# Optimization experiments

Measured on AMD Instinct MI355X. Metric: run time of the kernel, lower is better.

## Reference

```python
import jax, jax.numpy as jnp
import numpy as np

N_NODES = 50000
N_EDGES = 1600000
IN_FEATS = 128
HIDDEN = 128
N_CLASSES = 16
N_GRAPHS = 512


def setup_inputs() -> dict:
    key = jax.random.key(0)
    ks = jax.random.split(key, 10)
    features = jax.random.normal(ks[0], (N_NODES, IN_FEATS), dtype=jnp.float32)
    src = jax.random.randint(ks[1], (N_EDGES,), 0, N_NODES, dtype=jnp.int32)
    dst = jax.random.randint(ks[2], (N_EDGES,), 0, N_NODES, dtype=jnp.int32)
    graph_ids = jnp.sort(jax.random.randint(ks[3], (N_NODES,), 0, N_GRAPHS, dtype=jnp.int32))
    # GraphConv weights (glorot-ish scaling) and biases
    W1 = jax.random.normal(ks[4], (IN_FEATS, HIDDEN), dtype=jnp.float32) / np.sqrt(IN_FEATS)
    b1 = jnp.zeros((HIDDEN,), dtype=jnp.float32)
    W2 = jax.random.normal(ks[5], (HIDDEN, HIDDEN), dtype=jnp.float32) / np.sqrt(HIDDEN)
    b2 = jnp.zeros((HIDDEN,), dtype=jnp.float32)
    Wf = jax.random.normal(ks[6], (HIDDEN, N_CLASSES), dtype=jnp.float32) / np.sqrt(HIDDEN)
    bf = jnp.zeros((N_CLASSES,), dtype=jnp.float32)
    return {"features": features, "W1": W1, "b1": b1, "W2": W2, "b2": b2,
            "Wf": Wf, "bf": bf, "src": src, "dst": dst, "graph_ids": graph_ids}


def _graph_conv(h, W, b, src, dst, norm_out, norm_in):
    # DGL GraphConv, norm='both': h' = D_in^{-1/2} * A^T * (D_out^{-1/2} * h) @ W + b
    h = h * norm_out[:, None]              # [N, d] scale by src out-degree
    agg = jax.ops.segment_sum(h[src], dst, num_segments=N_NODES)  # gather-scatter SpMM
    agg = agg * norm_in[:, None]
    return agg @ W + b


def reference(features, W1, b1, W2, b2, Wf, bf, src, dst, graph_ids):
    ones_e = jnp.ones((N_EDGES,), dtype=features.dtype)
    deg_out = jax.ops.segment_sum(ones_e, src, num_segments=N_NODES)
    deg_in = jax.ops.segment_sum(ones_e, dst, num_segments=N_NODES)
    norm_out = jnp.where(deg_out > 0, jax.lax.rsqrt(jnp.maximum(deg_out, 1.0)), 0.0)
    norm_in = jnp.where(deg_in > 0, jax.lax.rsqrt(jnp.maximum(deg_in, 1.0)), 0.0)

    x = jax.nn.relu(_graph_conv(features, W1, b1, src, dst, norm_out, norm_in))
    x = jax.nn.relu(_graph_conv(x, W2, b2, src, dst, norm_out, norm_in))

    # mean_nodes: per-graph mean pooling over batched graph
    sums = jax.ops.segment_sum(x, graph_ids, num_segments=N_GRAPHS)   # [G, d]
    counts = jax.ops.segment_sum(jnp.ones((N_NODES,), dtype=x.dtype), graph_ids,
                                 num_segments=N_GRAPHS)
    pooled = sums / jnp.maximum(counts, 1.0)[:, None]
    return pooled @ Wf + bf
```

## Files before the change

### kernel.cpp

```cpp
#include <hip/hip_runtime.h>

#define N_NODES 50000
#define N_EDGES 1600000
#define FEATS 128
#define N_GRAPHS 512
#define N_CLASSES 16

#define NC 400
#define CE 4000
#define NB 391
#define SLAB 4608
#define CSLAB 5632
#define ZROW 50000
#define SRC_MID 25000

typedef __attribute__((ext_vector_type(8))) short bf16x8;
typedef __attribute__((ext_vector_type(4))) float f32x4;

__device__ inline unsigned bf16_rne_bits(float x) {
    unsigned u = __float_as_uint(x);
    return (u + 0x7FFFu + ((u >> 16) & 1u)) >> 16;
}
__device__ inline unsigned pack_bf16(float a, float b) {
    return (bf16_rne_bits(b) << 16) | bf16_rne_bits(a);
}
__device__ inline float bf16lo(unsigned u) { return __uint_as_float(u << 16); }
__device__ inline float bf16hi(unsigned u) { return __uint_as_float(u & 0xFFFF0000u); }

__global__ __launch_bounds__(256) void countrank_kernel(
        const int* __restrict__ src, const int* __restrict__ dst,
        unsigned* __restrict__ cntD, unsigned* __restrict__ cntS,
        const float* __restrict__ W1, const float* __restrict__ W2,
        unsigned short* __restrict__ t1h, unsigned short* __restrict__ t1l,
        unsigned short* __restrict__ t2h, unsigned short* __restrict__ t2l,
        int* __restrict__ gboth) {
    __shared__ unsigned hD[NB], hS[NB];
    if (blockIdx.x >= NC) {
        int b = blockIdx.x - NC;
        if (b == 0) {
#pragma unroll
            for (int i = 0; i < 4; ++i) gboth[threadIdx.x + 256 * i] = 0;
        }
        const float* W = (b < 64) ? W1 : W2;
        unsigned short* th = (b < 64) ? t1h : t2h;
        unsigned short* tl = (b < 64) ? t1l : t2l;
        int idx = (b & 63) * 256 + threadIdx.x;
        int k = idx >> 7;
        int col = idx & 127;
        float w = W[idx];
        unsigned hb = bf16_rne_bits(w);
        float hf = __uint_as_float(hb << 16);
        unsigned lb = bf16_rne_bits(w - hf);
        th[col * 128 + k] = (unsigned short)hb;
        tl[col * 128 + k] = (unsigned short)lb;
        return;
    }
    for (int i = threadIdx.x; i < NB; i += 256) { hD[i] = 0; hS[i] = 0; }
    __syncthreads();
    int c = blockIdx.x;
    int lo = c * CE;
    for (int i = lo + threadIdx.x; i < lo + CE; i += 256) {
        atomicAdd(&hD[dst[i] >> 7], 1u);
        atomicAdd(&hS[src[i] >> 7], 1u);
    }
    __syncthreads();
    for (int i = threadIdx.x; i < NB; i += 256) {
        cntD[c * NB + i] = hD[i];
        cntS[c * NB + i] = hS[i];
    }
}

__global__ __launch_bounds__(512) void colscan_kernel(
        unsigned* __restrict__ cntD, unsigned* __restrict__ cntS,
        unsigned* __restrict__ totD, unsigned* __restrict__ totS) {
    int bb = blockIdx.x;
    unsigned* cnt = (bb < NB) ? cntD : cntS;
    unsigned* tot = (bb < NB) ? totD : totS;
    int col = (bb < NB) ? bb : bb - NB;
    __shared__ unsigned buf[512];
    int t = threadIdx.x;
    unsigned v = (t < NC) ? cnt[t * NB + col] : 0;
    buf[t] = v;
    __syncthreads();
    for (int off = 1; off < 512; off <<= 1) {
        unsigned add = (t >= off) ? buf[t - off] : 0;
        __syncthreads();
        buf[t] += add;
        __syncthreads();
    }
    if (t < NC) cnt[t * NB + col] = buf[t] - v;
    if (t == NC - 1) tot[col] = buf[t];
}

__global__ __launch_bounds__(256) void scatter_kernel(
        const int* __restrict__ src, const int* __restrict__ dst,
        const unsigned* __restrict__ colbaseD, const unsigned* __restrict__ colbaseS,
        unsigned* __restrict__ arenaD, unsigned char* __restrict__ arenaS) {
    __shared__ unsigned cbD[NB], cbS[NB];
    int c = blockIdx.x;
    for (int i = threadIdx.x; i < NB; i += 256) {
        cbD[i] = colbaseD[c * NB + i];
        cbS[i] = colbaseS[c * NB + i];
    }
    __syncthreads();
    int lo = c * CE;
    for (int i = lo + threadIdx.x; i < lo + CE; i += 256) {
        int d = dst[i];
        int s = src[i];
        unsigned rD = atomicAdd(&cbD[d >> 7], 1u);
        arenaD[(unsigned)(d >> 7) * SLAB + rD] = (unsigned)s | ((unsigned)(d & 127) << 16);
        unsigned rS = atomicAdd(&cbS[s >> 7], 1u);
        arenaS[(unsigned)(s >> 7) * SLAB + rS] = (unsigned char)(s & 127);
    }
}

__global__ __launch_bounds__(256) void finalize_kernel(
        const unsigned* __restrict__ arenaD, const unsigned* __restrict__ totD,
        const unsigned char* __restrict__ arenaS, const unsigned* __restrict__ totS,
        unsigned short* __restrict__ csr, unsigned* __restrict__ row_start,
        unsigned* __restrict__ cnt2,
        const float* __restrict__ X, unsigned* __restrict__ Xs,
        float* __restrict__ norm_in_a, float* __restrict__ norm_out_a,
        const int* __restrict__ gids, int* __restrict__ gstart, int* __restrict__ gend) {
    int b = blockIdx.x;
    __shared__ unsigned hlo[128], hhi[128], clo[128], chi[128], loc[128], sbuf[128], degs[128];
    __shared__ unsigned short stag[CSLAB];
    int t = threadIdx.x;
    if (t < 128) { hlo[t] = 0; hhi[t] = 0; clo[t] = 0; chi[t] = 0; }
    for (int i = t; i < CSLAB; i += 256) stag[i] = (unsigned short)ZROW;
    __syncthreads();
    unsigned nbS = totS[b];
    const unsigned char* slabS = arenaS + (size_t)b * SLAB;
    for (unsigned i = t; i < nbS; i += 256) atomicAdd(&clo[slabS[i]], 1u);
    __syncthreads();
    if (t < 128) { degs[t] = clo[t]; clo[t] = 0; }
    __syncthreads();
    unsigned nb = totD[b];
    const unsigned* slab = arenaD + (size_t)b * SLAB;
    for (unsigned i = t; i < nb; i += 256) {
        unsigned e = slab[i];
        if ((e & 0xFFFFu) < SRC_MID) atomicAdd(&hlo[e >> 16], 1u);
        else atomicAdd(&hhi[e >> 16], 1u);
    }
    __syncthreads();
    unsigned myv = 0;
    if (t < 128) {
        myv = ((hlo[t] + 7u) & ~7u) + ((hhi[t] + 7u) & ~7u);
        sbuf[t] = myv;
    }
    __syncthreads();
    for (int off = 1; off < 128; off <<= 1) {
        unsigned add = 0;
        if (t < 128 && t >= off) add = sbuf[t - off];
        __syncthreads();
        if (t < 128) sbuf[t] += add;
        __syncthreads();
    }
    if (t < 128) {
        loc[t] = sbuf[t] - myv;
        int dd = b * 128 + t;
        if (dd < N_NODES) {
            cnt2[dd] = hlo[t] | (hhi[t] << 16);
            row_start[dd] = (unsigned)b * CSLAB + loc[t];
        }
    }
    __syncthreads();
    for (unsigned i = t; i < nb; i += 256) {
        unsigned e = slab[i];
        unsigned dl = e >> 16;
        unsigned s = e & 0xFFFFu;
        unsigned pos;
        if (s < SRC_MID) pos = loc[dl] + atomicAdd(&clo[dl], 1u);
        else pos = loc[dl] + ((hlo[dl] + 7u) & ~7u) + atomicAdd(&chi[dl], 1u);
        stag[pos] = (unsigned short)s;
    }
    __syncthreads();
    unsigned tot_aligned = sbuf[127];
    unsigned short* g = csr + (size_t)b * CSLAB;
    for (unsigned i = t; i < tot_aligned; i += 256) g[i] = stag[i];
    for (int task = t; task < 128 * 16; task += 256) {
        int nl = task >> 4;
        int c = task & 15;
        int node = b * 128 + nl;
        if (node < N_NODES) {
            unsigned d0 = degs[nl];
            float no = d0 > 0 ? rsqrtf((float)d0) : 0.f;
            float4 a0 = *reinterpret_cast<const float4*>(X + (size_t)node * FEATS + c * 8);
            float4 a1 = *reinterpret_cast<const float4*>(X + (size_t)node * FEATS + c * 8 + 4);
            uint4 p;
            p.x = pack_bf16(a0.x * no, a0.y * no);
            p.y = pack_bf16(a0.z * no, a0.w * no);
            p.z = pack_bf16(a1.x * no, a1.y * no);
            p.w = pack_bf16(a1.z * no, a1.w * no);
            *reinterpret_cast<uint4*>(Xs + (size_t)node * (FEATS / 2) + c * 4) = p;
        } else if (node == ZROW) {
            uint4 z = {0u, 0u, 0u, 0u};
            *reinterpret_cast<uint4*>(Xs + (size_t)node * (FEATS / 2) + c * 4) = z;
        }
    }
    if (t < 128) {
        int node = b * 128 + t;
        if (node < N_NODES) {
            unsigned d0 = degs[t];
            norm_out_a[node] = d0 > 0 ? rsqrtf((float)d0) : 0.f;
            unsigned d1 = hlo[t] + hhi[t];
            norm_in_a[node] = d1 > 0 ? rsqrtf((float)d1) : 0.f;
            int g2 = gids[node];
            if (node == 0 || gids[node - 1] != g2) gstart[g2] = node;
            if (node == N_NODES - 1 || gids[node + 1] != g2) gend[g2] = node + 1;
        }
    }
}

__global__ __launch_bounds__(256) void agg_kernel(const unsigned* __restrict__ Xs,
        const unsigned short* __restrict__ csr, const unsigned* __restrict__ row_start,
        const unsigned* __restrict__ cnt2, unsigned* __restrict__ out) {
    int b = blockIdx.x;
    int h = b & 1;
    int node = (b >> 1) * 8 + (threadIdx.x >> 5);
    if (node >= N_NODES) return;
    int lane = threadIdx.x & 31;
    unsigned c2 = cnt2[node];
    unsigned ntot = (((c2 & 0xFFFFu) + 7u) & ~7u) + (((c2 >> 16) + 7u) & ~7u);
    const unsigned short* row = csr + row_start[node];
    const unsigned base = h * 32 + lane;
    float alo = 0.f, ahi = 0.f;
#pragma unroll 2
    for (unsigned j = 0; j < ntot; j += 8) {
        uint4 iv = *reinterpret_cast<const uint4*>(row + j);
        unsigned s0 = iv.x & 0xFFFFu, s1 = iv.x >> 16;
        unsigned s2 = iv.y & 0xFFFFu, s3 = iv.y >> 16;
        unsigned s4 = iv.z & 0xFFFFu, s5 = iv.z >> 16;
        unsigned s6 = iv.w & 0xFFFFu, s7 = iv.w >> 16;
        unsigned g0 = Xs[(size_t)s0 * 64 + base];
        unsigned g1 = Xs[(size_t)s1 * 64 + base];
        unsigned g2 = Xs[(size_t)s2 * 64 + base];
        unsigned g3 = Xs[(size_t)s3 * 64 + base];
        unsigned g4 = Xs[(size_t)s4 * 64 + base];
        unsigned g5 = Xs[(size_t)s5 * 64 + base];
        unsigned g6 = Xs[(size_t)s6 * 64 + base];
        unsigned g7 = Xs[(size_t)s7 * 64 + base];
        alo += ((bf16lo(g0) + bf16lo(g1)) + (bf16lo(g2) + bf16lo(g3)))
             + ((bf16lo(g4) + bf16lo(g5)) + (bf16lo(g6) + bf16lo(g7)));
        ahi += ((bf16hi(g0) + bf16hi(g1)) + (bf16hi(g2) + bf16hi(g3)))
             + ((bf16hi(g4) + bf16hi(g5)) + (bf16hi(g6) + bf16hi(g7)));
    }
    out[(size_t)node * 64 + base] = pack_bf16(alo, ahi);
}

template <bool BF16_OUT>
__global__ __launch_bounds__(256) void gemm_kernel(
        const unsigned* __restrict__ A,
        const unsigned short* __restrict__ Wth, const unsigned short* __restrict__ Wtl,
        const float* __restrict__ bias, const float* __restrict__ norm_in,
        const float* __restrict__ post, float* __restrict__ out_f32,
        unsigned short* __restrict__ out_b16, int n_rows) {
    __shared__ unsigned sWh[128 * 68];
    __shared__ unsigned sWl[128 * 68];
    {
        const uint4* gh = reinterpret_cast<const uint4*>(Wth);
        const uint4* gl = reinterpret_cast<const uint4*>(Wtl);
        for (int i = threadIdx.x; i < 2048; i += 256) {
            int col = i >> 4, q = i & 15;
            *reinterpret_cast<uint4*>(sWh + col * 68 + q * 4) = gh[i];
            *reinterpret_cast<uint4*>(sWl + col * 68 + q * 4) = gl[i];
        }
    }
    __syncthreads();

    const int l = threadIdx.x & 63;
    const int w = threadIdx.x >> 6;
    const int rl = l & 15;
    const int kg = l >> 4;
    const int row0 = blockIdx.x * 64 + w * 16;

    int row_a = row0 + rl;
    if (row_a >= n_rows) row_a = n_rows - 1;
    const uint4* Arow = reinterpret_cast<const uint4*>(A + (size_t)row_a * 64);

    f32x4 acc[8];
#pragma unroll
    for (int ct = 0; ct < 8; ++ct) acc[ct] = (f32x4){0.f, 0.f, 0.f, 0.f};

#pragma unroll
    for (int s = 0; s < 4; ++s) {
        bf16x8 af = __builtin_bit_cast(bf16x8, Arow[4 * s + kg]);
#pragma unroll
        for (int ct = 0; ct < 8; ++ct) {
            int colb = ct * 16 + rl;
            bf16x8 bh = __builtin_bit_cast(bf16x8,
                *reinterpret_cast<const uint4*>(sWh + colb * 68 + 16 * s + 4 * kg));
            bf16x8 bl = __builtin_bit_cast(bf16x8,
                *reinterpret_cast<const uint4*>(sWl + colb * 68 + 16 * s + 4 * kg));
            acc[ct] = __builtin_amdgcn_mfma_f32_16x16x32_bf16(af, bl, acc[ct], 0, 0, 0);
            acc[ct] = __builtin_amdgcn_mfma_f32_16x16x32_bf16(af, bh, acc[ct], 0, 0, 0);
        }
    }

    const int rb = row0 + kg * 4;
    float ni[4], po[4];
#pragma unroll
    for (int j = 0; j < 4; ++j) {
        int r = rb + j;
        bool v = r < n_rows;
        ni[j] = v ? norm_in[r] : 0.f;
        po[j] = (BF16_OUT && v && post) ? post[r] : 1.f;
    }
#pragma unroll
    for (int ct = 0; ct < 8; ++ct) {
        int col = ct * 16 + rl;
        float bc = bias[col];
#pragma unroll
        for (int j = 0; j < 4; ++j) {
            int r = rb + j;
            if (r < n_rows) {
                float o = fmaxf(fmaf(acc[ct][j], ni[j], bc), 0.f);
                if (BF16_OUT)
                    out_b16[(size_t)r * 128 + col] = (unsigned short)bf16_rne_bits(o * po[j]);
                else
                    out_f32[(size_t)r * 128 + col] = o;
            }
        }
    }
}

__global__ __launch_bounds__(256) void pool_final_kernel(
        const unsigned short* __restrict__ H, const int* __restrict__ gstart,
        const int* __restrict__ gend, const float* __restrict__ Wf,
        const float* __restrict__ bf, float* __restrict__ out) {
    int g = blockIdx.x;
    int s = gstart[g];
    int e = gend[g];
    int f = threadIdx.x & 127;
    int h = threadIdx.x >> 7;
    float acc = 0.f;
    for (int r = s + h; r < e; r += 2)
        acc += __uint_as_float((unsigned)H[(size_t)r * FEATS + f] << 16);
    __shared__ float tmp[256];
    __shared__ float pooled[FEATS];
    tmp[threadIdx.x] = acc;
    __syncthreads();
    if (threadIdx.x < FEATS) {
        float inv = 1.0f / fmaxf((float)(e - s), 1.0f);
        pooled[threadIdx.x] = (tmp[threadIdx.x] + tmp[threadIdx.x + 128]) * inv;
    }
    __syncthreads();
    if (threadIdx.x < N_CLASSES) {
        int c = threadIdx.x;
        float d = bf[c];
        for (int k = 0; k < FEATS; ++k) d = fmaf(pooled[k], Wf[k * N_CLASSES + c], d);
        out[g * N_CLASSES + c] = d;
    }
}

extern "C" void kernel_launch(void* const* d_in, const int* in_sizes, int n_in,
                              void* d_out, int out_size, void* d_ws, size_t ws_size,
                              hipStream_t stream) {
    const float* features = (const float*)d_in[0];
    const float* W1 = (const float*)d_in[1];
    const float* b1 = (const float*)d_in[2];
    const float* W2 = (const float*)d_in[3];
    const float* b2 = (const float*)d_in[4];
    const float* Wf = (const float*)d_in[5];
    const float* bf = (const float*)d_in[6];
    const int* src = (const int*)d_in[7];
    const int* dst = (const int*)d_in[8];
    const int* gids = (const int*)d_in[9];
    float* out = (float*)d_out;

    char* wp = (char*)d_ws;
    auto alloc = [&wp](size_t bytes) {
        char* p = wp;
        wp += (bytes + 255) & ~(size_t)255;
        return p;
    };
    unsigned* buf0u = (unsigned*)alloc(((size_t)N_NODES + 1) * 64 * 4);
    float* buf1 = (float*)alloc((size_t)N_NODES * FEATS * 4 + 256);
    unsigned* B16 = (unsigned*)buf1;
    unsigned short* B16s = (unsigned short*)buf1;
    float* norm_in_a = (float*)alloc(N_NODES * 4);
    float* norm_out_a = (float*)alloc(N_NODES * 4);
    unsigned* cnt2 = (unsigned*)alloc(N_NODES * 4);
    unsigned* row_start = (unsigned*)alloc(N_NODES * 4);
    int* gboth = (int*)alloc(2 * N_GRAPHS * 4);
    int* gstart = gboth;
    int* gend = gboth + N_GRAPHS;
    unsigned short* t1h = (unsigned short*)alloc(4 * 16384 * 2);
    unsigned short* t1l = t1h + 16384;
    unsigned short* t2h = t1l + 16384;
    unsigned short* t2l = t2h + 16384;
    unsigned* cntD = (unsigned*)alloc((size_t)NC * NB * 4);
    unsigned* cntS = (unsigned*)alloc((size_t)NC * NB * 4);
    unsigned* totD = (unsigned*)alloc(NB * 4);
    unsigned* totS = (unsigned*)alloc(NB * 4);
    unsigned* arenaD = (unsigned*)alloc((size_t)NB * SLAB * 4);
    unsigned short* csr = (unsigned short*)alloc((size_t)NB * CSLAB * 2);
    unsigned char* arenaS = (unsigned char*)alloc((size_t)NB * SLAB);

    countrank_kernel<<<NC + 128, 256, 0, stream>>>(src, dst, cntD, cntS,
                                                   W1, W2, t1h, t1l, t2h, t2l, gboth);
    colscan_kernel<<<2 * NB, 512, 0, stream>>>(cntD, cntS, totD, totS);
    scatter_kernel<<<NC, 256, 0, stream>>>(src, dst, cntD, cntS, arenaD, arenaS);
    finalize_kernel<<<NB, 256, 0, stream>>>(arenaD, totD, arenaS, totS,
                                            csr, row_start, cnt2,
                                            features, B16, norm_in_a, norm_out_a,
                                            gids, gstart, gend);

    const int agg_blocks = 2 * ((N_NODES + 7) / 8);
    const int gemm_blocks = (N_NODES + 63) / 64;

    agg_kernel<<<agg_blocks, 256, 0, stream>>>(B16, csr, row_start, cnt2, buf0u);
    gemm_kernel<true><<<gemm_blocks, 256, 0, stream>>>(
        buf0u, t1h, t1l, b1, norm_in_a, norm_out_a, nullptr, B16s, N_NODES);

    agg_kernel<<<agg_blocks, 256, 0, stream>>>(B16, csr, row_start, cnt2, buf0u);
    gemm_kernel<true><<<gemm_blocks, 256, 0, stream>>>(
        buf0u, t2h, t2l, b2, norm_in_a, nullptr, nullptr, B16s, N_NODES);

    pool_final_kernel<<<N_GRAPHS, 256, 0, stream>>>(B16s, gstart, gend, Wf, bf, out);
}
```

Baseline: 216.7 us.

## Split bf16 node features into four 32-feature planes for narrower gathers

Stores the normalized bf16 feature matrix and GEMM outputs in four planar slabs of 32 features each instead of row-major 128-wide rows. The aggregation kernel now assigns 16 lanes per node per plane and gathers 64-byte segments from one plane, and the pooling kernel reads the planar layout. This aims to improve cache locality of the random neighbor gathers, at the cost of more CSR index reads per feature and strided output stores in the GEMM epilogue. The unused fp32 output path of the GEMM template is removed.

```diff
diff --git a/kernel.cpp b/kernel.cpp
--- a/kernel.cpp
+++ b/kernel.cpp
@@ -13,6 +13,9 @@
 #define CSLAB 5632
 #define ZROW 50000
 #define SRC_MID 25000
+#define PHS 50048
+#define PHU ((size_t)PHS * 16)
+#define PHH ((size_t)PHS * 32)
 
 typedef __attribute__((ext_vector_type(8))) short bf16x8;
 typedef __attribute__((ext_vector_type(4))) float f32x4;
@@ -182,6 +185,7 @@
         int nl = task >> 4;
         int c = task & 15;
         int node = b * 128 + nl;
+        unsigned* dstp = Xs + (size_t)(c >> 2) * PHU + (size_t)node * 16 + (c & 3) * 4;
         if (node < N_NODES) {
             unsigned d0 = degs[nl];
             float no = d0 > 0 ? rsqrtf((float)d0) : 0.f;
@@ -192,10 +196,10 @@
             p.y = pack_bf16(a0.z * no, a0.w * no);
             p.z = pack_bf16(a1.x * no, a1.y * no);
             p.w = pack_bf16(a1.z * no, a1.w * no);
-            *reinterpret_cast<uint4*>(Xs + (size_t)node * (FEATS / 2) + c * 4) = p;
+            *reinterpret_cast<uint4*>(dstp) = p;
         } else if (node == ZROW) {
             uint4 z = {0u, 0u, 0u, 0u};
-            *reinterpret_cast<uint4*>(Xs + (size_t)node * (FEATS / 2) + c * 4) = z;
+            *reinterpret_cast<uint4*>(dstp) = z;
         }
     }
     if (t < 128) {
@@ -216,14 +220,14 @@
         const unsigned short* __restrict__ csr, const unsigned* __restrict__ row_start,
         const unsigned* __restrict__ cnt2, unsigned* __restrict__ out) {
     int b = blockIdx.x;
-    int h = b & 1;
-    int node = (b >> 1) * 8 + (threadIdx.x >> 5);
+    int p = b & 3;
+    int node = (b >> 2) * 16 + (threadIdx.x >> 4);
     if (node >= N_NODES) return;
-    int lane = threadIdx.x & 31;
+    int lane = threadIdx.x & 15;
     unsigned c2 = cnt2[node];
     unsigned ntot = (((c2 & 0xFFFFu) + 7u) & ~7u) + (((c2 >> 16) + 7u) & ~7u);
     const unsigned short* row = csr + row_start[node];
-    const unsigned base = h * 32 + lane;
+    const unsigned* __restrict__ Xp = Xs + (size_t)p * PHU;
     float alo = 0.f, ahi = 0.f;
 #pragma unroll 2
     for (unsigned j = 0; j < ntot; j += 8) {
@@ -232,29 +236,28 @@
         unsigned s2 = iv.y & 0xFFFFu, s3 = iv.y >> 16;
         unsigned s4 = iv.z & 0xFFFFu, s5 = iv.z >> 16;
         unsigned s6 = iv.w & 0xFFFFu, s7 = iv.w >> 16;
-        unsigned g0 = Xs[(size_t)s0 * 64 + base];
-        unsigned g1 = Xs[(size_t)s1 * 64 + base];
-        unsigned g2 = Xs[(size_t)s2 * 64 + base];
-        unsigned g3 = Xs[(size_t)s3 * 64 + base];
-        unsigned g4 = Xs[(size_t)s4 * 64 + base];
-        unsigned g5 = Xs[(size_t)s5 * 64 + base];
-        unsigned g6 = Xs[(size_t)s6 * 64 + base];
-        unsigned g7 = Xs[(size_t)s7 * 64 + base];
+        unsigned g0 = Xp[(size_t)s0 * 16 + lane];
+        unsigned g1 = Xp[(size_t)s1 * 16 + lane];
+        unsigned g2 = Xp[(size_t)s2 * 16 + lane];
+        unsigned g3 = Xp[(size_t)s3 * 16 + lane];
+        unsigned g4 = Xp[(size_t)s4 * 16 + lane];
+        unsigned g5 = Xp[(size_t)s5 * 16 + lane];
+        unsigned g6 = Xp[(size_t)s6 * 16 + lane];
+        unsigned g7 = Xp[(size_t)s7 * 16 + lane];
         alo += ((bf16lo(g0) + bf16lo(g1)) + (bf16lo(g2) + bf16lo(g3)))
              + ((bf16lo(g4) + bf16lo(g5)) + (bf16lo(g6) + bf16lo(g7)));
         ahi += ((bf16hi(g0) + bf16hi(g1)) + (bf16hi(g2) + bf16hi(g3)))
              + ((bf16hi(g4) + bf16hi(g5)) + (bf16hi(g6) + bf16hi(g7)));
     }
-    out[(size_t)node * 64 + base] = pack_bf16(alo, ahi);
-}
-
-template <bool BF16_OUT>
+    out[(size_t)node * 64 + p * 16 + lane] = pack_bf16(alo, ahi);
+}
+
 __global__ __launch_bounds__(256) void gemm_kernel(
         const unsigned* __restrict__ A,
         const unsigned short* __restrict__ Wth, const unsigned short* __restrict__ Wtl,
         const float* __restrict__ bias, const float* __restrict__ norm_in,
-        const float* __restrict__ post, float* __restrict__ out_f32,
-        unsigned short* __restrict__ out_b16, int n_rows) {
+        const float* __restrict__ post, unsigned short* __restrict__ out_b16,
+        int n_rows) {
     __shared__ unsigned sWh[128 * 68];
     __shared__ unsigned sWl[128 * 68];
     {
@@ -304,21 +307,19 @@
         int r = rb + j;
         bool v = r < n_rows;
         ni[j] = v ? norm_in[r] : 0.f;
-        po[j] = (BF16_OUT && v && post) ? post[r] : 1.f;
+        po[j] = (v && post) ? post[r] : 1.f;
     }
 #pragma unroll
     for (int ct = 0; ct < 8; ++ct) {
         int col = ct * 16 + rl;
         float bc = bias[col];
+        unsigned short* outp = out_b16 + (size_t)(col >> 5) * PHH + (col & 31);
 #pragma unroll
         for (int j = 0; j < 4; ++j) {
             int r = rb + j;
             if (r < n_rows) {
                 float o = fmaxf(fmaf(acc[ct][j], ni[j], bc), 0.f);
-                if (BF16_OUT)
-                    out_b16[(size_t)r * 128 + col] = (unsigned short)bf16_rne_bits(o * po[j]);
-                else
-                    out_f32[(size_t)r * 128 + col] = o;
+                outp[(size_t)r * 32] = (unsigned short)bf16_rne_bits(o * po[j]);
             }
         }
     }
@@ -333,9 +334,10 @@
     int e = gend[g];
     int f = threadIdx.x & 127;
     int h = threadIdx.x >> 7;
+    const unsigned short* Hp = H + (size_t)(f >> 5) * PHH + (f & 31);
     float acc = 0.f;
     for (int r = s + h; r < e; r += 2)
-        acc += __uint_as_float((unsigned)H[(size_t)r * FEATS + f] << 16);
+        acc += __uint_as_float((unsigned)Hp[(size_t)r * 32] << 16);
     __shared__ float tmp[256];
     __shared__ float pooled[FEATS];
     tmp[threadIdx.x] = acc;
@@ -375,9 +377,8 @@
         return p;
     };
     unsigned* buf0u = (unsigned*)alloc(((size_t)N_NODES + 1) * 64 * 4);
-    float* buf1 = (float*)alloc((size_t)N_NODES * FEATS * 4 + 256);
-    unsigned* B16 = (unsigned*)buf1;
-    unsigned short* B16s = (unsigned short*)buf1;
+    unsigned* B16 = (unsigned*)alloc(4 * PHU * 4);
+    unsigned short* B16s = (unsigned short*)B16;
     float* norm_in_a = (float*)alloc(N_NODES * 4);
     float* norm_out_a = (float*)alloc(N_NODES * 4);
     unsigned* cnt2 = (unsigned*)alloc(N_NODES * 4);
@@ -406,16 +407,16 @@
                                             features, B16, norm_in_a, norm_out_a,
                                             gids, gstart, gend);
 
-    const int agg_blocks = 2 * ((N_NODES + 7) / 8);
+    const int agg_blocks = 4 * ((N_NODES + 15) / 16);
     const int gemm_blocks = (N_NODES + 63) / 64;
 
     agg_kernel<<<agg_blocks, 256, 0, stream>>>(B16, csr, row_start, cnt2, buf0u);
-    gemm_kernel<true><<<gemm_blocks, 256, 0, stream>>>(
-        buf0u, t1h, t1l, b1, norm_in_a, norm_out_a, nullptr, B16s, N_NODES);
+    gemm_kernel<<<gemm_blocks, 256, 0, stream>>>(
+        buf0u, t1h, t1l, b1, norm_in_a, norm_out_a, B16s, N_NODES);
 
     agg_kernel<<<agg_blocks, 256, 0, stream>>>(B16, csr, row_start, cnt2, buf0u);
-    gemm_kernel<true><<<gemm_blocks, 256, 0, stream>>>(
-        buf0u, t2h, t2l, b2, norm_in_a, nullptr, nullptr, B16s, N_NODES);
+    gemm_kernel<<<gemm_blocks, 256, 0, stream>>>(
+        buf0u, t2h, t2l, b2, norm_in_a, nullptr, B16s, N_NODES);
 
     pool_final_kernel<<<N_GRAPHS, 256, 0, stream>>>(B16s, gstart, gend, Wf, bf, out);
 }
```

Measured after the change: 227.9 us. 1.05x slower.
